# Kernel optimization log

Measured on AMD Instinct MI355X. Metric: run time of the kernel, lower is better.

## Reference

```python
import jax, jax.numpy as jnp
import numpy as np

LN_EPS = 1e-5


def _layer_norm(x, w, b, eps=LN_EPS):
    mu = jnp.mean(x, axis=-1, keepdims=True)
    var = jnp.var(x, axis=-1, keepdims=True)
    return (x - mu) * jax.lax.rsqrt(var + eps) * w + b


def setup_inputs() -> dict:
    key = jax.random.key(0)
    ks = jax.random.split(key, 6)
    H, I, B, S = 1024, 4096, 4, 2048
    return {
        "x": jax.random.normal(ks[0], (B, S, H), jnp.float32),
        "ln_weight": jnp.ones((H,), jnp.float32),
        "ln_bias": jnp.zeros((H,), jnp.float32),
        "i2h_weight": jax.random.normal(ks[1], (2 * I, H), jnp.float32) * 0.02,
        "i2h_bias": jax.random.normal(ks[2], (2 * I,), jnp.float32) * 0.02,
        "h2o_weight": jax.random.normal(ks[3], (H, I), jnp.float32) * 0.02,
        "h2o_bias": jax.random.normal(ks[4], (H,), jnp.float32) * 0.02,
        "post_ln_weight": jnp.ones((H,), jnp.float32),
        "post_ln_bias": jnp.zeros((H,), jnp.float32),
    }


def reference(x, ln_weight, ln_bias, i2h_weight, i2h_bias, h2o_weight, h2o_bias,
              post_ln_weight, post_ln_bias):
    B, S, H = x.shape
    x2 = x.reshape(-1, H)  # [N, H]
    x_ln = _layer_norm(x2, ln_weight, ln_bias)
    # i2h: [N, 2I]
    pre = jnp.einsum('nh,oh->no', x_ln, i2h_weight) + i2h_bias
    I = pre.shape[-1] // 2
    pre_gate, lin = pre[:, :I], pre[:, I:]
    # gated gelu (tanh-approx, matching gelu_fused)
    hid = jax.nn.gelu(pre_gate, approximate=True) * lin
    out = jnp.einsum('ni,oi->no', hid, h2o_weight) + h2o_bias
    out = _layer_norm(out, post_ln_weight, post_ln_bias)
    out = out + x2  # residual (dropout=0)
    return out.reshape(B, S, H)
```

## Files before the change

kernel.cpp:

```cpp
#include <hip/hip_runtime.h>
#include <stdint.h>

#define N_ROWS 8192
#define H_DIM  1024
#define I_DIM  4096

typedef unsigned short u16;
typedef __bf16 bf16x8 __attribute__((ext_vector_type(8)));
typedef float f32x4 __attribute__((ext_vector_type(4)));
typedef u16 u16x4 __attribute__((ext_vector_type(4)));

#define BAR()   asm volatile("s_barrier" ::: "memory")
#define LGKM0() do { asm volatile("s_waitcnt lgkmcnt(0)" ::: "memory"); __builtin_amdgcn_sched_barrier(0); } while (0)
#define VMW(n)  do { asm volatile("s_waitcnt vmcnt(" #n ")" ::: "memory"); __builtin_amdgcn_sched_barrier(0); } while (0)

__device__ __forceinline__ u16 f2bf(float f) {
    union { float f; uint32_t u; } v; v.f = f;
    uint32_t u = v.u;
    u += 0x7FFFu + ((u >> 16) & 1u);
    return (u16)(u >> 16);
}

__device__ __forceinline__ float bf2f(u16 h) {
    union { uint32_t u; float f; } v; v.u = ((uint32_t)h) << 16;
    return v.f;
}

__device__ __forceinline__ float gelu_tanh(float x) {
    float u = 0.7978845608028654f * (x + 0.044715f * x * x * x);
    u = fminf(fmaxf(u, -15.f), 15.f);
    float e = __expf(2.f * u);
    float t = (e - 1.f) / (e + 1.f);
    return 0.5f * x * (1.f + t);
}

__device__ __forceinline__ void load_lds16(const void* g, void* l) {
    auto gp = reinterpret_cast<const __attribute__((address_space(1))) uint32_t*>(
        reinterpret_cast<uintptr_t>(g));
    auto lp = reinterpret_cast<__attribute__((address_space(3))) uint32_t*>(
        static_cast<uint32_t>(reinterpret_cast<uintptr_t>(l)));
    __builtin_amdgcn_global_load_lds(gp, lp, 16, 0, 0);
}

__global__ __launch_bounds__(512, 2) void gemm1_gated(
    const u16* __restrict__ A, const u16* __restrict__ W,
    const float* __restrict__ bias, u16* __restrict__ hid)
{
    __shared__ u16 lds[2 * 32768];
    const int t = threadIdx.x;
    const int lane = t & 63, wid = t >> 6;
    const int wm = wid >> 2, wn = wid & 3;
    const int g = lane >> 4, r16 = lane & 15;

    const int brow = blockIdx.y * 256;
    const int bcol = blockIdx.x * 128;

    const int tr = t >> 2;
    const int swz8 = ((t & 3) ^ ((t >> 3) & 3)) * 8;
    const u16* pA  = A + (size_t)(brow + tr) * H_DIM + swz8;
    const u16* pBg = W + (size_t)(bcol + tr) * H_DIM + swz8;
    const u16* pBl = W + (size_t)(I_DIM + bcol + tr) * H_DIM + swz8;
    const int dst = t * 8;

    const int sl    = (g ^ ((r16 >> 1) & 3)) * 8;
    const int rdA   = (wm * 128 + r16) * 32 + sl;
    const int rdBg  = 16384 + (wn * 32 + r16) * 32 + sl;
    const int rdBl  = rdBg + 4096;

    f32x4 accg[8][2] = {};
    f32x4 accl[8][2] = {};

#pragma unroll
    for (int s = 0; s < 2; ++s) {
        load_lds16(pA + s * 32,                 lds + s * 8192 + dst);
        load_lds16(pA + 128 * H_DIM + s * 32,   lds + s * 8192 + 4096 + dst);
        load_lds16(pBg + s * 32,                lds + 16384 + s * 8192 + dst);
        load_lds16(pBl + s * 32,                lds + 16384 + s * 8192 + 4096 + dst);
    }
    VMW(4); BAR();

    const int NT = H_DIM / 64;
    for (int kt = 0; kt < NT; ++kt) {
        const u16* lA = lds + (kt & 1) * 32768;
        u16* dS = lds + ((kt & 1) ^ 1) * 32768;
        const bool st = (kt + 1 < NT);
        const int k1 = (kt + 1) * 64;
        const bool tail = (kt == NT - 1);

#pragma unroll
        for (int ks = 0; ks < 2; ++ks) {
            bf16x8 af[8], bg[2], bl[2];
#pragma unroll
            for (int m = 0; m < 8; ++m) af[m] = *(const bf16x8*)(lA + ks * 8192 + rdA + m * 512);
#pragma unroll
            for (int n = 0; n < 2; ++n) {
                bg[n] = *(const bf16x8*)(lA + ks * 8192 + rdBg + n * 512);
                bl[n] = *(const bf16x8*)(lA + ks * 8192 + rdBl + n * 512);
            }
            if (st) {
                load_lds16(pA + k1 + ks * 32,               dS + ks * 8192 + dst);
                load_lds16(pA + 128 * H_DIM + k1 + ks * 32, dS + ks * 8192 + 4096 + dst);
                load_lds16(pBg + k1 + ks * 32,              dS + 16384 + ks * 8192 + dst);
                load_lds16(pBl + k1 + ks * 32,              dS + 16384 + ks * 8192 + 4096 + dst);
            }
            if (tail) { VMW(0); } else { VMW(4); }
            BAR(); LGKM0();
            __builtin_amdgcn_s_setprio(1);
#pragma unroll
            for (int m = 0; m < 8; ++m)
#pragma unroll
                for (int n = 0; n < 2; ++n) {
                    accg[m][n] = __builtin_amdgcn_mfma_f32_16x16x32_bf16(af[m], bg[n], accg[m][n], 0, 0, 0);
                    accl[m][n] = __builtin_amdgcn_mfma_f32_16x16x32_bf16(af[m], bl[n], accl[m][n], 0, 0, 0);
                }
            __builtin_amdgcn_s_setprio(0);
            BAR();
        }
    }

#pragma unroll
    for (int n = 0; n < 2; ++n) {
        const int cg = bcol + wn * 32 + n * 16 + r16;
        const float bgv = bias[cg], blv = bias[I_DIM + cg];
#pragma unroll
        for (int m = 0; m < 8; ++m) {
            const int row = brow + wm * 128 + m * 16 + g * 4;
            u16* hp = hid + (size_t)row * I_DIM + cg;
#pragma unroll
            for (int r = 0; r < 4; ++r) {
                float gate = accg[m][n][r] + bgv;
                float lin  = accl[m][n][r] + blv;
                hp[(size_t)r * I_DIM] = f2bf(gelu_tanh(gate) * lin);
            }
        }
    }
}

__global__ __launch_bounds__(512, 2) void gemm2_k(
    const u16* __restrict__ A, const u16* __restrict__ W,
    const float* __restrict__ bias, u16* __restrict__ opb)
{
    __shared__ u16 lds[2 * 24576];
    const int t = threadIdx.x;
    const int lane = t & 63, wid = t >> 6;
    const int wm = wid >> 1, wn = wid & 1;
    const int g = lane >> 4, r16 = lane & 15;

    const int brow = blockIdx.y * 256;
    const int bcol = blockIdx.x * 128;

    const int tr = t >> 2;
    const int swz8 = ((t & 3) ^ ((t >> 3) & 3)) * 8;
    const u16* pA = A + (size_t)(brow + tr) * I_DIM + swz8;
    const u16* pB = W + (size_t)(bcol + tr) * I_DIM + swz8;
    const int dst = t * 8;

    const int sl   = (g ^ ((r16 >> 1) & 3)) * 8;
    const int rdA  = (wm * 64 + r16) * 32 + sl;
    const int rdB  = 16384 + (wn * 64 + r16) * 32 + sl;

    f32x4 acc[4][4] = {};

#pragma unroll
    for (int s = 0; s < 2; ++s) {
        load_lds16(pA + s * 32,               lds + s * 8192 + dst);
        load_lds16(pA + 128 * I_DIM + s * 32, lds + s * 8192 + 4096 + dst);
        load_lds16(pB + s * 32,               lds + 16384 + s * 4096 + dst);
    }
    VMW(3); BAR();

    const int NT = I_DIM / 64;
    for (int kt = 0; kt < NT; ++kt) {
        const u16* lA = lds + (kt & 1) * 24576;
        u16* dS = lds + ((kt & 1) ^ 1) * 24576;
        const bool st = (kt + 1 < NT);
        const int k1 = (kt + 1) * 64;
        const bool tail = (kt == NT - 1);

#pragma unroll
        for (int ks = 0; ks < 2; ++ks) {
            bf16x8 af[4], bf[4];
#pragma unroll
            for (int m = 0; m < 4; ++m) af[m] = *(const bf16x8*)(lA + ks * 8192 + rdA + m * 512);
#pragma unroll
            for (int n = 0; n < 4; ++n) bf[n] = *(const bf16x8*)(lA + ks * 4096 + rdB + n * 512);
            if (st) {
                load_lds16(pA + k1 + ks * 32,               dS + ks * 8192 + dst);
                load_lds16(pA + 128 * I_DIM + k1 + ks * 32, dS + ks * 8192 + 4096 + dst);
                load_lds16(pB + k1 + ks * 32,               dS + 16384 + ks * 4096 + dst);
            }
            if (tail) { VMW(0); } else { VMW(3); }
            BAR(); LGKM0();
            __builtin_amdgcn_s_setprio(1);
#pragma unroll
            for (int m = 0; m < 4; ++m)
#pragma unroll
                for (int n = 0; n < 4; ++n)
                    acc[m][n] = __builtin_amdgcn_mfma_f32_16x16x32_bf16(af[m], bf[n], acc[m][n], 0, 0, 0);
            __builtin_amdgcn_s_setprio(0);
            BAR();
        }
    }

#pragma unroll
    for (int n = 0; n < 4; ++n) {
        const int cg = bcol + wn * 64 + n * 16 + r16;
        const float bv = bias[cg];
#pragma unroll
        for (int m = 0; m < 4; ++m) {
            const int row = brow + wm * 64 + m * 16 + g * 4;
            u16* op = opb + (size_t)row * H_DIM + cg;
#pragma unroll
            for (int r = 0; r < 4; ++r)
                op[(size_t)r * H_DIM] = f2bf(acc[m][n][r] + bv);
        }
    }
}

__device__ __forceinline__ void block_mean_var(float s, float s2, float* red, int t,
                                               float& mu, float& var) {
#pragma unroll
    for (int off = 32; off > 0; off >>= 1) {
        s  += __shfl_down(s, off);
        s2 += __shfl_down(s2, off);
    }
    const int wid = t >> 6;
    if ((t & 63) == 0) { red[wid] = s; red[4 + wid] = s2; }
    __syncthreads();
    if (t == 0) {
        float a = red[0] + red[1] + red[2] + red[3];
        float b = red[4] + red[5] + red[6] + red[7];
        red[0] = a * (1.f / H_DIM);
        red[1] = b * (1.f / H_DIM);
    }
    __syncthreads();
    mu = red[0];
    var = red[1] - mu * mu;
}

__global__ void ln_pre(const float* __restrict__ x, const float* __restrict__ w,
                       const float* __restrict__ b, u16* __restrict__ xln)
{
    __shared__ float red[8];
    const int row = blockIdx.x, t = threadIdx.x;
    const float4 v = reinterpret_cast<const float4*>(x + (size_t)row * H_DIM)[t];
    float mu, var;
    block_mean_var(v.x + v.y + v.z + v.w,
                   v.x * v.x + v.y * v.y + v.z * v.z + v.w * v.w, red, t, mu, var);
    const float rstd = rsqrtf(var + 1e-5f);
    const float4 wv = reinterpret_cast<const float4*>(w)[t];
    const float4 bv = reinterpret_cast<const float4*>(b)[t];
    u16x4 o;
    o.x = f2bf((v.x - mu) * rstd * wv.x + bv.x);
    o.y = f2bf((v.y - mu) * rstd * wv.y + bv.y);
    o.z = f2bf((v.z - mu) * rstd * wv.z + bv.z);
    o.w = f2bf((v.w - mu) * rstd * wv.w + bv.w);
    reinterpret_cast<u16x4*>(xln + (size_t)row * H_DIM)[t] = o;
}

__global__ void ln_post_res(const u16* __restrict__ op, const float* __restrict__ w,
                            const float* __restrict__ b, const float* __restrict__ x,
                            float* __restrict__ out)
{
    __shared__ float red[8];
    const int row = blockIdx.x, t = threadIdx.x;
    const u16x4 hv = reinterpret_cast<const u16x4*>(op + (size_t)row * H_DIM)[t];
    float4 v;
    v.x = bf2f(hv.x); v.y = bf2f(hv.y); v.z = bf2f(hv.z); v.w = bf2f(hv.w);
    float mu, var;
    block_mean_var(v.x + v.y + v.z + v.w,
                   v.x * v.x + v.y * v.y + v.z * v.z + v.w * v.w, red, t, mu, var);
    const float rstd = rsqrtf(var + 1e-5f);
    const float4 wv = reinterpret_cast<const float4*>(w)[t];
    const float4 bv = reinterpret_cast<const float4*>(b)[t];
    const float4 xv = reinterpret_cast<const float4*>(x + (size_t)row * H_DIM)[t];
    float4 o;
    o.x = (v.x - mu) * rstd * wv.x + bv.x + xv.x;
    o.y = (v.y - mu) * rstd * wv.y + bv.y + xv.y;
    o.z = (v.z - mu) * rstd * wv.z + bv.z + xv.z;
    o.w = (v.w - mu) * rstd * wv.w + bv.w + xv.w;
    reinterpret_cast<float4*>(out + (size_t)row * H_DIM)[t] = o;
}

__global__ void cvt_bf16(const float* __restrict__ in, u16* __restrict__ out, int n4) {
    int i = blockIdx.x * blockDim.x + threadIdx.x;
    if (i >= n4) return;
    float4 v = reinterpret_cast<const float4*>(in)[i];
    u16x4 o = { f2bf(v.x), f2bf(v.y), f2bf(v.z), f2bf(v.w) };
    reinterpret_cast<u16x4*>(out)[i] = o;
}

extern "C" void kernel_launch(void* const* d_in, const int* in_sizes, int n_in,
                              void* d_out, int out_size, void* d_ws, size_t ws_size,
                              hipStream_t stream)
{
    const float* x   = (const float*)d_in[0];
    const float* lnw = (const float*)d_in[1];
    const float* lnb = (const float*)d_in[2];
    const float* w1  = (const float*)d_in[3];
    const float* b1  = (const float*)d_in[4];
    const float* w2  = (const float*)d_in[5];
    const float* b2  = (const float*)d_in[6];
    const float* pw  = (const float*)d_in[7];
    const float* pb  = (const float*)d_in[8];
    float* out = (float*)d_out;

    char* ws = (char*)d_ws;
    u16* xln = (u16*)(ws);
    u16* w1b = (u16*)(ws + (16u << 20));
    u16* hid = (u16*)(ws + (32u << 20));
    u16* w2b = (u16*)(ws);
    u16* opb = (u16*)(ws + (8u << 20));

    cvt_bf16<<<(2 * I_DIM * H_DIM / 4 + 255) / 256, 256, 0, stream>>>(w1, w1b, 2 * I_DIM * H_DIM / 4);
    ln_pre<<<N_ROWS, 256, 0, stream>>>(x, lnw, lnb, xln);
    gemm1_gated<<<dim3(I_DIM / 128, N_ROWS / 256), 512, 0, stream>>>(xln, w1b, b1, hid);
    cvt_bf16<<<(H_DIM * I_DIM / 4 + 255) / 256, 256, 0, stream>>>(w2, w2b, H_DIM * I_DIM / 4);
    gemm2_k<<<dim3(H_DIM / 128, N_ROWS / 256), 512, 0, stream>>>(hid, w2b, b2, opb);
    ln_post_res<<<N_ROWS, 256, 0, stream>>>(opb, pw, pb, x, out);
}
```

Measured before the change: 276.9 us.

## Deepen GEMM prefetch pipelines to multi-stage LDS ring buffers

Both GEMM kernels move from double-buffered 64-wide K steps to 32-wide K stages in a ring of LDS buffers: four stages with three in flight for gemm1, five stages with four in flight for gemm2. gemm1 also interleaves the gate and linear weight rows into one B tile and splits each stage into two MFMA phases, so A and B prefetches are issued at separate points. The aim is to hide more global-load latency behind MFMA work. In exchange it adds more barriers per K element and more complex vmcnt bookkeeping near the tail.

After: 274.9 us. About the same (-0.7%).

```diff
diff --git a/kernel.cpp b/kernel.cpp
--- a/kernel.cpp
+++ b/kernel.cpp
@@ -46,7 +46,7 @@
     const u16* __restrict__ A, const u16* __restrict__ W,
     const float* __restrict__ bias, u16* __restrict__ hid)
 {
-    __shared__ u16 lds[2 * 32768];
+    __shared__ u16 lds[4 * 16384];
     const int t = threadIdx.x;
     const int lane = t & 63, wid = t >> 6;
     const int wm = wid >> 2, wn = wid & 3;
@@ -57,65 +57,80 @@
 
     const int tr = t >> 2;
     const int swz8 = ((t & 3) ^ ((t >> 3) & 3)) * 8;
-    const u16* pA  = A + (size_t)(brow + tr) * H_DIM + swz8;
-    const u16* pBg = W + (size_t)(bcol + tr) * H_DIM + swz8;
-    const u16* pBl = W + (size_t)(I_DIM + bcol + tr) * H_DIM + swz8;
+    const u16* pA = A + (size_t)(brow + tr) * H_DIM + swz8;
+    const int j0 = tr, j1 = tr + 128;
+    const int cj0 = bcol + (j0 >> 6) * 32 + (j0 & 31);
+    const int cj1 = bcol + (j1 >> 6) * 32 + (j1 & 31);
+    const int gr0 = ((j0 & 63) < 32) ? cj0 : (I_DIM + cj0);
+    const int gr1 = ((j1 & 63) < 32) ? cj1 : (I_DIM + cj1);
+    const u16* pB0 = W + (size_t)gr0 * H_DIM + swz8;
+    const u16* pB1 = W + (size_t)gr1 * H_DIM + swz8;
     const int dst = t * 8;
 
-    const int sl    = (g ^ ((r16 >> 1) & 3)) * 8;
-    const int rdA   = (wm * 128 + r16) * 32 + sl;
-    const int rdBg  = 16384 + (wn * 32 + r16) * 32 + sl;
-    const int rdBl  = rdBg + 4096;
+    const int sl  = (g ^ ((r16 >> 1) & 3)) * 8;
+    const int rdA = (wm * 128 + r16) * 32 + sl;
+    const int rdB = 8192 + (wn * 64 + r16) * 32 + sl;
 
     f32x4 accg[8][2] = {};
     f32x4 accl[8][2] = {};
 
 #pragma unroll
-    for (int s = 0; s < 2; ++s) {
-        load_lds16(pA + s * 32,                 lds + s * 8192 + dst);
-        load_lds16(pA + 128 * H_DIM + s * 32,   lds + s * 8192 + 4096 + dst);
-        load_lds16(pBg + s * 32,                lds + 16384 + s * 8192 + dst);
-        load_lds16(pBl + s * 32,                lds + 16384 + s * 8192 + 4096 + dst);
-    }
-    VMW(4); BAR();
-
-    const int NT = H_DIM / 64;
+    for (int p = 0; p < 3; ++p) {
+        u16* S = lds + p * 16384;
+        load_lds16(pA + p * 32,                        S + dst);
+        load_lds16(pA + (size_t)128 * H_DIM + p * 32,  S + 4096 + dst);
+        load_lds16(pB0 + p * 32,                       S + 8192 + dst);
+        load_lds16(pB1 + p * 32,                       S + 12288 + dst);
+    }
+    VMW(8); BAR();
+
+    int bc = 0, bs = 3;
+    const int NT = H_DIM / 32;
     for (int kt = 0; kt < NT; ++kt) {
-        const u16* lA = lds + (kt & 1) * 32768;
-        u16* dS = lds + ((kt & 1) ^ 1) * 32768;
-        const bool st = (kt + 1 < NT);
-        const int k1 = (kt + 1) * 64;
-        const bool tail = (kt == NT - 1);
-
-#pragma unroll
-        for (int ks = 0; ks < 2; ++ks) {
-            bf16x8 af[8], bg[2], bl[2];
-#pragma unroll
-            for (int m = 0; m < 8; ++m) af[m] = *(const bf16x8*)(lA + ks * 8192 + rdA + m * 512);
-#pragma unroll
-            for (int n = 0; n < 2; ++n) {
-                bg[n] = *(const bf16x8*)(lA + ks * 8192 + rdBg + n * 512);
-                bl[n] = *(const bf16x8*)(lA + ks * 8192 + rdBl + n * 512);
-            }
-            if (st) {
-                load_lds16(pA + k1 + ks * 32,               dS + ks * 8192 + dst);
-                load_lds16(pA + 128 * H_DIM + k1 + ks * 32, dS + ks * 8192 + 4096 + dst);
-                load_lds16(pBg + k1 + ks * 32,              dS + 16384 + ks * 8192 + dst);
-                load_lds16(pBl + k1 + ks * 32,              dS + 16384 + ks * 8192 + 4096 + dst);
-            }
-            if (tail) { VMW(0); } else { VMW(4); }
-            BAR(); LGKM0();
-            __builtin_amdgcn_s_setprio(1);
-#pragma unroll
-            for (int m = 0; m < 8; ++m)
-#pragma unroll
-                for (int n = 0; n < 2; ++n) {
-                    accg[m][n] = __builtin_amdgcn_mfma_f32_16x16x32_bf16(af[m], bg[n], accg[m][n], 0, 0, 0);
-                    accl[m][n] = __builtin_amdgcn_mfma_f32_16x16x32_bf16(af[m], bl[n], accl[m][n], 0, 0, 0);
-                }
-            __builtin_amdgcn_s_setprio(0);
-            BAR();
-        }
+        const u16* L = lds + bc * 16384;
+        u16* S = lds + bs * 16384;
+        const bool st = (kt + 3 < NT);
+        const int kG = (kt + 3) * 32;
+        bf16x8 af[8], bb[2];
+
+        if (st) {
+            load_lds16(pA + kG,                        S + dst);
+            load_lds16(pA + (size_t)128 * H_DIM + kG,  S + 4096 + dst);
+        }
+#pragma unroll
+        for (int m = 0; m < 8; ++m) af[m] = *(const bf16x8*)(L + rdA + m * 512);
+#pragma unroll
+        for (int n = 0; n < 2; ++n) bb[n] = *(const bf16x8*)(L + rdB + n * 512);
+        BAR(); LGKM0();
+        __builtin_amdgcn_s_setprio(1);
+#pragma unroll
+        for (int m = 0; m < 8; ++m)
+#pragma unroll
+            for (int n = 0; n < 2; ++n)
+                accg[m][n] = __builtin_amdgcn_mfma_f32_16x16x32_bf16(af[m], bb[n], accg[m][n], 0, 0, 0);
+        __builtin_amdgcn_s_setprio(0);
+        BAR();
+
+        if (st) {
+            load_lds16(pB0 + kG, S + 8192 + dst);
+            load_lds16(pB1 + kG, S + 12288 + dst);
+        }
+#pragma unroll
+        for (int n = 0; n < 2; ++n) bb[n] = *(const bf16x8*)(L + rdB + 1024 + n * 512);
+        BAR(); LGKM0();
+        __builtin_amdgcn_s_setprio(1);
+#pragma unroll
+        for (int m = 0; m < 8; ++m)
+#pragma unroll
+            for (int n = 0; n < 2; ++n)
+                accl[m][n] = __builtin_amdgcn_mfma_f32_16x16x32_bf16(af[m], bb[n], accl[m][n], 0, 0, 0);
+        __builtin_amdgcn_s_setprio(0);
+        if (kt < NT - 3)      { VMW(8); }
+        else if (kt == NT - 3){ VMW(4); }
+        else                  { VMW(0); }
+        BAR();
+        bc = (bc + 1) & 3;
+        bs = (bs + 1) & 3;
     }
 
 #pragma unroll
@@ -140,7 +155,7 @@
     const u16* __restrict__ A, const u16* __restrict__ W,
     const float* __restrict__ bias, u16* __restrict__ opb)
 {
-    __shared__ u16 lds[2 * 24576];
+    __shared__ u16 lds[5 * 12288];
     const int t = threadIdx.x;
     const int lane = t & 63, wid = t >> 6;
     const int wm = wid >> 1, wn = wid & 1;
@@ -155,51 +170,52 @@
     const u16* pB = W + (size_t)(bcol + tr) * I_DIM + swz8;
     const int dst = t * 8;
 
-    const int sl   = (g ^ ((r16 >> 1) & 3)) * 8;
-    const int rdA  = (wm * 64 + r16) * 32 + sl;
-    const int rdB  = 16384 + (wn * 64 + r16) * 32 + sl;
+    const int sl  = (g ^ ((r16 >> 1) & 3)) * 8;
+    const int rdA = (wm * 64 + r16) * 32 + sl;
+    const int rdB = 8192 + (wn * 64 + r16) * 32 + sl;
 
     f32x4 acc[4][4] = {};
 
 #pragma unroll
-    for (int s = 0; s < 2; ++s) {
-        load_lds16(pA + s * 32,               lds + s * 8192 + dst);
-        load_lds16(pA + 128 * I_DIM + s * 32, lds + s * 8192 + 4096 + dst);
-        load_lds16(pB + s * 32,               lds + 16384 + s * 4096 + dst);
-    }
-    VMW(3); BAR();
-
-    const int NT = I_DIM / 64;
+    for (int p = 0; p < 4; ++p) {
+        u16* S = lds + p * 12288;
+        load_lds16(pA + p * 32,                        S + dst);
+        load_lds16(pA + (size_t)128 * I_DIM + p * 32,  S + 4096 + dst);
+        load_lds16(pB + p * 32,                        S + 8192 + dst);
+    }
+    VMW(9); BAR();
+
+    int bc = 0, bs = 4;
+    const int NT = I_DIM / 32;
     for (int kt = 0; kt < NT; ++kt) {
-        const u16* lA = lds + (kt & 1) * 24576;
-        u16* dS = lds + ((kt & 1) ^ 1) * 24576;
-        const bool st = (kt + 1 < NT);
-        const int k1 = (kt + 1) * 64;
-        const bool tail = (kt == NT - 1);
-
-#pragma unroll
-        for (int ks = 0; ks < 2; ++ks) {
-            bf16x8 af[4], bf[4];
-#pragma unroll
-            for (int m = 0; m < 4; ++m) af[m] = *(const bf16x8*)(lA + ks * 8192 + rdA + m * 512);
-#pragma unroll
-            for (int n = 0; n < 4; ++n) bf[n] = *(const bf16x8*)(lA + ks * 4096 + rdB + n * 512);
-            if (st) {
-                load_lds16(pA + k1 + ks * 32,               dS + ks * 8192 + dst);
-                load_lds16(pA + 128 * I_DIM + k1 + ks * 32, dS + ks * 8192 + 4096 + dst);
-                load_lds16(pB + k1 + ks * 32,               dS + 16384 + ks * 4096 + dst);
-            }
-            if (tail) { VMW(0); } else { VMW(3); }
-            BAR(); LGKM0();
-            __builtin_amdgcn_s_setprio(1);
-#pragma unroll
-            for (int m = 0; m < 4; ++m)
-#pragma unroll
-                for (int n = 0; n < 4; ++n)
-                    acc[m][n] = __builtin_amdgcn_mfma_f32_16x16x32_bf16(af[m], bf[n], acc[m][n], 0, 0, 0);
-            __builtin_amdgcn_s_setprio(0);
-            BAR();
-        }
+        const u16* L = lds + bc * 12288;
+        u16* S = lds + bs * 12288;
+        if (kt + 4 < NT) {
+            const int kG = (kt + 4) * 32;
+            load_lds16(pA + kG,                        S + dst);
+            load_lds16(pA + (size_t)128 * I_DIM + kG,  S + 4096 + dst);
+            load_lds16(pB + kG,                        S + 8192 + dst);
+        }
+        bf16x8 af[4], bf[4];
+#pragma unroll
+        for (int m = 0; m < 4; ++m) af[m] = *(const bf16x8*)(L + rdA + m * 512);
+#pragma unroll
+        for (int n = 0; n < 4; ++n) bf[n] = *(const bf16x8*)(L + rdB + n * 512);
+        BAR(); LGKM0();
+        __builtin_amdgcn_s_setprio(1);
+#pragma unroll
+        for (int m = 0; m < 4; ++m)
+#pragma unroll
+            for (int n = 0; n < 4; ++n)
+                acc[m][n] = __builtin_amdgcn_mfma_f32_16x16x32_bf16(af[m], bf[n], acc[m][n], 0, 0, 0);
+        __builtin_amdgcn_s_setprio(0);
+        if (kt < NT - 4)      { VMW(9); }
+        else if (kt == NT - 4){ VMW(6); }
+        else if (kt == NT - 3){ VMW(3); }
+        else                  { VMW(0); }
+        BAR();
+        bc = (bc == 4) ? 0 : bc + 1;
+        bs = (bs == 4) ? 0 : bs + 1;
     }
 
 #pragma unroll
```

## Restructure GEMM main loops into 8-phase pipelined schedule with interleaved gate/linear tiles

Applied to the files above, without the earlier changes.

Both GEMM kernels now unroll two K-tiles per iteration into eight small phases. Each phase issues a slice of the next global-to-LDS stages, reads a half-set of fragments and runs a smaller MFMA batch. The aim is finer-grained overlap of memory traffic, LDS reads and matrix math, plus lower register pressure. GEMM1 interleaves gate and linear weight rows in the B tile so each wave computes a single 8x4 accumulator set, with gate and linear sitting in columns n and n+2. The patch also drops the sched_barrier from the wait macros and changes the LDS swizzle formula. The cost is many more barriers per K step and delicate vmcnt bookkeeping.

New measurement: 270.7 us. 2.2% less time.

```diff
diff --git a/kernel.cpp b/kernel.cpp
--- a/kernel.cpp
+++ b/kernel.cpp
@@ -11,8 +11,8 @@
 typedef u16 u16x4 __attribute__((ext_vector_type(4)));
 
 #define BAR()   asm volatile("s_barrier" ::: "memory")
-#define LGKM0() do { asm volatile("s_waitcnt lgkmcnt(0)" ::: "memory"); __builtin_amdgcn_sched_barrier(0); } while (0)
-#define VMW(n)  do { asm volatile("s_waitcnt vmcnt(" #n ")" ::: "memory"); __builtin_amdgcn_sched_barrier(0); } while (0)
+#define LGKM0() asm volatile("s_waitcnt lgkmcnt(0)" ::: "memory")
+#define VMW(n)  asm volatile("s_waitcnt vmcnt(" #n ")" ::: "memory")
 
 __device__ __forceinline__ u16 f2bf(float f) {
     union { float f; uint32_t u; } v; v.f = f;
@@ -56,67 +56,106 @@
     const int bcol = blockIdx.x * 128;
 
     const int tr = t >> 2;
-    const int swz8 = ((t & 3) ^ ((t >> 3) & 3)) * 8;
-    const u16* pA  = A + (size_t)(brow + tr) * H_DIM + swz8;
-    const u16* pBg = W + (size_t)(bcol + tr) * H_DIM + swz8;
-    const u16* pBl = W + (size_t)(I_DIM + bcol + tr) * H_DIM + swz8;
+    const int swz8 = ((t & 3) ^ ((tr >> 1) & 3)) * 8;
+    const u16* pA = A + (size_t)(brow + tr) * H_DIM + swz8;
+    const int j0 = tr, j1 = tr + 128;
+    const int c0 = bcol + ((j0 >> 6) << 5) + (j0 & 31);
+    const int c1 = bcol + ((j1 >> 6) << 5) + (j1 & 31);
+    const u16* pB0 = W + (size_t)(((j0 & 63) < 32) ? c0 : (I_DIM + c0)) * H_DIM + swz8;
+    const u16* pB1 = W + (size_t)(((j1 & 63) < 32) ? c1 : (I_DIM + c1)) * H_DIM + swz8;
     const int dst = t * 8;
 
-    const int sl    = (g ^ ((r16 >> 1) & 3)) * 8;
-    const int rdA   = (wm * 128 + r16) * 32 + sl;
-    const int rdBg  = 16384 + (wn * 32 + r16) * 32 + sl;
-    const int rdBl  = rdBg + 4096;
-
-    f32x4 accg[8][2] = {};
-    f32x4 accl[8][2] = {};
-
-#pragma unroll
-    for (int s = 0; s < 2; ++s) {
-        load_lds16(pA + s * 32,                 lds + s * 8192 + dst);
-        load_lds16(pA + 128 * H_DIM + s * 32,   lds + s * 8192 + 4096 + dst);
-        load_lds16(pBg + s * 32,                lds + 16384 + s * 8192 + dst);
-        load_lds16(pBl + s * 32,                lds + 16384 + s * 8192 + 4096 + dst);
-    }
+    const int sl  = (g ^ ((r16 >> 1) & 3)) * 8;
+    const int rdA = (wm * 128 + r16) * 32 + sl;
+    const int rdB = 16384 + (wn * 64 + r16) * 32 + sl;
+
+    f32x4 acc[8][4] = {};
+
+    u16* const B0 = lds;
+    u16* const B1 = lds + 32768;
+
+#define STG_A1(S, kk, ks) do { \
+    load_lds16(pA + (kk) + (ks) * 32,                       (S) + (ks) * 8192 + dst); \
+    load_lds16(pA + (size_t)128 * H_DIM + (kk) + (ks) * 32, (S) + (ks) * 8192 + 4096 + dst); } while (0)
+#define STG_B1(S, kk, ks) do { \
+    load_lds16(pB0 + (kk) + (ks) * 32, (S) + 16384 + (ks) * 8192 + dst); \
+    load_lds16(pB1 + (kk) + (ks) * 32, (S) + 16384 + (ks) * 8192 + 4096 + dst); } while (0)
+#define RD_A1(L, ks, mh) { _Pragma("unroll") for (int m = 0; m < 4; ++m) \
+    af[m] = *(const bf16x8*)((L) + (ks) * 8192 + rdA + ((mh) * 4 + m) * 512); }
+#define RD_B1(L, ks) { _Pragma("unroll") for (int n = 0; n < 4; ++n) \
+    bf[n] = *(const bf16x8*)((L) + (ks) * 8192 + rdB + n * 512); }
+#define MM1(mh) { _Pragma("unroll") for (int m = 0; m < 4; ++m) _Pragma("unroll") for (int n = 0; n < 4; ++n) \
+    acc[(mh) * 4 + m][n] = __builtin_amdgcn_mfma_f32_16x16x32_bf16(af[m], bf[n], acc[(mh) * 4 + m][n], 0, 0, 0); }
+
+    STG_A1(B0, 0, 0); STG_B1(B0, 0, 0);
+    STG_A1(B0, 0, 1); STG_B1(B0, 0, 1);
+    STG_A1(B1, 64, 0); STG_B1(B1, 64, 0);
     VMW(4); BAR();
 
-    const int NT = H_DIM / 64;
-    for (int kt = 0; kt < NT; ++kt) {
-        const u16* lA = lds + (kt & 1) * 32768;
-        u16* dS = lds + ((kt & 1) ^ 1) * 32768;
-        const bool st = (kt + 1 < NT);
-        const int k1 = (kt + 1) * 64;
-        const bool tail = (kt == NT - 1);
-
-#pragma unroll
-        for (int ks = 0; ks < 2; ++ks) {
-            bf16x8 af[8], bg[2], bl[2];
-#pragma unroll
-            for (int m = 0; m < 8; ++m) af[m] = *(const bf16x8*)(lA + ks * 8192 + rdA + m * 512);
-#pragma unroll
-            for (int n = 0; n < 2; ++n) {
-                bg[n] = *(const bf16x8*)(lA + ks * 8192 + rdBg + n * 512);
-                bl[n] = *(const bf16x8*)(lA + ks * 8192 + rdBl + n * 512);
-            }
-            if (st) {
-                load_lds16(pA + k1 + ks * 32,               dS + ks * 8192 + dst);
-                load_lds16(pA + 128 * H_DIM + k1 + ks * 32, dS + ks * 8192 + 4096 + dst);
-                load_lds16(pBg + k1 + ks * 32,              dS + 16384 + ks * 8192 + dst);
-                load_lds16(pBl + k1 + ks * 32,              dS + 16384 + ks * 8192 + 4096 + dst);
-            }
-            if (tail) { VMW(0); } else { VMW(4); }
-            BAR(); LGKM0();
-            __builtin_amdgcn_s_setprio(1);
-#pragma unroll
-            for (int m = 0; m < 8; ++m)
-#pragma unroll
-                for (int n = 0; n < 2; ++n) {
-                    accg[m][n] = __builtin_amdgcn_mfma_f32_16x16x32_bf16(af[m], bg[n], accg[m][n], 0, 0, 0);
-                    accl[m][n] = __builtin_amdgcn_mfma_f32_16x16x32_bf16(af[m], bl[n], accl[m][n], 0, 0, 0);
-                }
-            __builtin_amdgcn_s_setprio(0);
-            BAR();
-        }
-    }
+    const int NI = H_DIM / 128;
+#pragma unroll 1
+    for (int it = 0; it < NI; ++it) {
+        const int kk1 = (2 * it + 1) * 64;
+        const int kk2 = (2 * it + 2) * 64;
+        const int kk3 = (2 * it + 3) * 64;
+        const bool s2 = (it + 1 < NI);
+        const bool last = (it == NI - 1);
+        bf16x8 af[4], bf[4];
+
+        STG_A1(B1, kk1, 1); STG_B1(B1, kk1, 1);
+        RD_A1(B0, 0, 0); RD_B1(B0, 0);
+        BAR(); LGKM0();
+        __builtin_amdgcn_s_setprio(1); MM1(0); __builtin_amdgcn_s_setprio(0);
+        BAR();
+
+        if (s2) STG_B1(B0, kk2, 0);
+        RD_A1(B0, 0, 1);
+        BAR(); LGKM0();
+        __builtin_amdgcn_s_setprio(1); MM1(1); __builtin_amdgcn_s_setprio(0);
+        BAR();
+
+        if (s2) STG_A1(B0, kk2, 0);
+        RD_A1(B0, 1, 0); RD_B1(B0, 1);
+        BAR(); LGKM0();
+        __builtin_amdgcn_s_setprio(1); MM1(0); __builtin_amdgcn_s_setprio(0);
+        BAR();
+
+        if (s2) STG_B1(B0, kk2, 1);
+        RD_A1(B0, 1, 1);
+        BAR(); LGKM0();
+        __builtin_amdgcn_s_setprio(1); MM1(1); __builtin_amdgcn_s_setprio(0);
+        if (last) { VMW(0); } else { VMW(6); }
+        BAR();
+
+        if (s2) STG_A1(B0, kk2, 1);
+        RD_A1(B1, 0, 0); RD_B1(B1, 0);
+        BAR(); LGKM0();
+        __builtin_amdgcn_s_setprio(1); MM1(0); __builtin_amdgcn_s_setprio(0);
+        BAR();
+
+        if (s2) STG_B1(B1, kk3, 0);
+        RD_A1(B1, 0, 1);
+        BAR(); LGKM0();
+        __builtin_amdgcn_s_setprio(1); MM1(1); __builtin_amdgcn_s_setprio(0);
+        BAR();
+
+        if (s2) STG_A1(B1, kk3, 0);
+        RD_A1(B1, 1, 0); RD_B1(B1, 1);
+        BAR(); LGKM0();
+        __builtin_amdgcn_s_setprio(1); MM1(0); __builtin_amdgcn_s_setprio(0);
+        BAR();
+
+        RD_A1(B1, 1, 1);
+        BAR(); LGKM0();
+        __builtin_amdgcn_s_setprio(1); MM1(1); __builtin_amdgcn_s_setprio(0);
+        if (last) { VMW(0); } else { VMW(4); }
+        BAR();
+    }
+#undef STG_A1
+#undef STG_B1
+#undef RD_A1
+#undef RD_B1
+#undef MM1
 
 #pragma unroll
     for (int n = 0; n < 2; ++n) {
@@ -128,8 +167,8 @@
             u16* hp = hid + (size_t)row * I_DIM + cg;
 #pragma unroll
             for (int r = 0; r < 4; ++r) {
-                float gate = accg[m][n][r] + bgv;
-                float lin  = accl[m][n][r] + blv;
+                float gate = acc[m][n][r] + bgv;
+                float lin  = acc[m][n + 2][r] + blv;
                 hp[(size_t)r * I_DIM] = f2bf(gelu_tanh(gate) * lin);
             }
         }
@@ -150,57 +189,101 @@
     const int bcol = blockIdx.x * 128;
 
     const int tr = t >> 2;
-    const int swz8 = ((t & 3) ^ ((t >> 3) & 3)) * 8;
+    const int swz8 = ((t & 3) ^ ((tr >> 1) & 3)) * 8;
     const u16* pA = A + (size_t)(brow + tr) * I_DIM + swz8;
     const u16* pB = W + (size_t)(bcol + tr) * I_DIM + swz8;
     const int dst = t * 8;
 
-    const int sl   = (g ^ ((r16 >> 1) & 3)) * 8;
-    const int rdA  = (wm * 64 + r16) * 32 + sl;
-    const int rdB  = 16384 + (wn * 64 + r16) * 32 + sl;
+    const int sl  = (g ^ ((r16 >> 1) & 3)) * 8;
+    const int rdA = (wm * 64 + r16) * 32 + sl;
+    const int rdB = 16384 + (wn * 64 + r16) * 32 + sl;
 
     f32x4 acc[4][4] = {};
 
-#pragma unroll
-    for (int s = 0; s < 2; ++s) {
-        load_lds16(pA + s * 32,               lds + s * 8192 + dst);
-        load_lds16(pA + 128 * I_DIM + s * 32, lds + s * 8192 + 4096 + dst);
-        load_lds16(pB + s * 32,               lds + 16384 + s * 4096 + dst);
-    }
+    u16* const B0 = lds;
+    u16* const B1 = lds + 24576;
+
+#define STG_A2(S, kk, ks) do { \
+    load_lds16(pA + (kk) + (ks) * 32,                       (S) + (ks) * 8192 + dst); \
+    load_lds16(pA + (size_t)128 * I_DIM + (kk) + (ks) * 32, (S) + (ks) * 8192 + 4096 + dst); } while (0)
+#define STG_B2(S, kk, ks) do { \
+    load_lds16(pB + (kk) + (ks) * 32, (S) + 16384 + (ks) * 4096 + dst); } while (0)
+#define RD_A2(L, ks, mh) { _Pragma("unroll") for (int m = 0; m < 2; ++m) \
+    af[m] = *(const bf16x8*)((L) + (ks) * 8192 + rdA + ((mh) * 2 + m) * 512); }
+#define RD_B2(L, ks) { _Pragma("unroll") for (int n = 0; n < 4; ++n) \
+    bf[n] = *(const bf16x8*)((L) + (ks) * 4096 + rdB + n * 512); }
+#define MM2(mh) { _Pragma("unroll") for (int m = 0; m < 2; ++m) _Pragma("unroll") for (int n = 0; n < 4; ++n) \
+    acc[(mh) * 2 + m][n] = __builtin_amdgcn_mfma_f32_16x16x32_bf16(af[m], bf[n], acc[(mh) * 2 + m][n], 0, 0, 0); }
+
+    STG_A2(B0, 0, 0); STG_B2(B0, 0, 0);
+    STG_A2(B0, 0, 1); STG_B2(B0, 0, 1);
+    STG_A2(B1, 64, 0); STG_B2(B1, 64, 0);
     VMW(3); BAR();
 
-    const int NT = I_DIM / 64;
-    for (int kt = 0; kt < NT; ++kt) {
-        const u16* lA = lds + (kt & 1) * 24576;
-        u16* dS = lds + ((kt & 1) ^ 1) * 24576;
-        const bool st = (kt + 1 < NT);
-        const int k1 = (kt + 1) * 64;
-        const bool tail = (kt == NT - 1);
-
-#pragma unroll
-        for (int ks = 0; ks < 2; ++ks) {
-            bf16x8 af[4], bf[4];
-#pragma unroll
-            for (int m = 0; m < 4; ++m) af[m] = *(const bf16x8*)(lA + ks * 8192 + rdA + m * 512);
-#pragma unroll
-            for (int n = 0; n < 4; ++n) bf[n] = *(const bf16x8*)(lA + ks * 4096 + rdB + n * 512);
-            if (st) {
-                load_lds16(pA + k1 + ks * 32,               dS + ks * 8192 + dst);
-                load_lds16(pA + 128 * I_DIM + k1 + ks * 32, dS + ks * 8192 + 4096 + dst);
-                load_lds16(pB + k1 + ks * 32,               dS + 16384 + ks * 4096 + dst);
-            }
-            if (tail) { VMW(0); } else { VMW(3); }
-            BAR(); LGKM0();
-            __builtin_amdgcn_s_setprio(1);
-#pragma unroll
-            for (int m = 0; m < 4; ++m)
-#pragma unroll
-                for (int n = 0; n < 4; ++n)
-                    acc[m][n] = __builtin_amdgcn_mfma_f32_16x16x32_bf16(af[m], bf[n], acc[m][n], 0, 0, 0);
-            __builtin_amdgcn_s_setprio(0);
-            BAR();
-        }
-    }
+    const int NI = I_DIM / 128;
+#pragma unroll 1
+    for (int it = 0; it < NI; ++it) {
+        const int kk1 = (2 * it + 1) * 64;
+        const int kk2 = (2 * it + 2) * 64;
+        const int kk3 = (2 * it + 3) * 64;
+        const bool s2 = (it + 1 < NI);
+        const bool last = (it == NI - 1);
+        bf16x8 af[2], bf[4];
+
+        STG_A2(B1, kk1, 1); STG_B2(B1, kk1, 1);
+        RD_A2(B0, 0, 0); RD_B2(B0, 0);
+        BAR(); LGKM0();
+        __builtin_amdgcn_s_setprio(1); MM2(0); __builtin_amdgcn_s_setprio(0);
+        BAR();
+
+        if (s2) STG_B2(B0, kk2, 0);
+        RD_A2(B0, 0, 1);
+        BAR(); LGKM0();
+        __builtin_amdgcn_s_setprio(1); MM2(1); __builtin_amdgcn_s_setprio(0);
+        BAR();
+
+        if (s2) STG_A2(B0, kk2, 0);
+        RD_A2(B0, 1, 0); RD_B2(B0, 1);
+        BAR(); LGKM0();
+        __builtin_amdgcn_s_setprio(1); MM2(0); __builtin_amdgcn_s_setprio(0);
+        BAR();
+
+        if (s2) STG_B2(B0, kk2, 1);
+        RD_A2(B0, 1, 1);
+        BAR(); LGKM0();
+        __builtin_amdgcn_s_setprio(1); MM2(1); __builtin_amdgcn_s_setprio(0);
+        if (last) { VMW(0); } else { VMW(4); }
+        BAR();
+
+        if (s2) STG_A2(B0, kk2, 1);
+        RD_A2(B1, 0, 0); RD_B2(B1, 0);
+        BAR(); LGKM0();
+        __builtin_amdgcn_s_setprio(1); MM2(0); __builtin_amdgcn_s_setprio(0);
+        BAR();
+
+        if (s2) STG_B2(B1, kk3, 0);
+        RD_A2(B1, 0, 1);
+        BAR(); LGKM0();
+        __builtin_amdgcn_s_setprio(1); MM2(1); __builtin_amdgcn_s_setprio(0);
+        BAR();
+
+        if (s2) STG_A2(B1, kk3, 0);
+        RD_A2(B1, 1, 0); RD_B2(B1, 1);
+        BAR(); LGKM0();
+        __builtin_amdgcn_s_setprio(1); MM2(0); __builtin_amdgcn_s_setprio(0);
+        BAR();
+
+        RD_A2(B1, 1, 1);
+        BAR(); LGKM0();
+        __builtin_amdgcn_s_setprio(1); MM2(1); __builtin_amdgcn_s_setprio(0);
+        if (last) { VMW(0); } else { VMW(3); }
+        BAR();
+    }
+#undef STG_A2
+#undef STG_B2
+#undef RD_A2
+#undef RD_B2
+#undef MM2
 
 #pragma unroll
     for (int n = 0; n < 4; ++n) {
```
